# Kernel optimization log

Hardware: AMD Instinct MI355X
Metric: run time of the kernel (lower is better)

The kernel has to match this reference:

```python
import jax, jax.numpy as jnp
import numpy as np

N = 32768      # total nodes
G = 64         # graphs
NPG = 512      # nodes per graph (equal-size graphs)
K = 256        # ceil(NPG * pooling_ratio), pooling_ratio=0.5
D = 256        # input_dim
H = 256        # hidden_dim
FD = 3 * H     # fusion dim
C = 10         # num_classes
E = 262144     # edges
EPS = 1e-5     # BatchNorm eps


def setup_inputs() -> dict:
    key = jax.random.key(0)
    ks = jax.random.split(key, 20)
    w = lambda k, s: jax.random.normal(k, s, jnp.float32) * 0.05
    inp = {
        'x': jax.random.normal(ks[0], (N, D), jnp.float32),
        'edge_index': jax.random.randint(ks[1], (2, E), 0, N, jnp.int64),
        'batch': (jnp.arange(N, dtype=jnp.int64) // NPG),
        'w_s1': w(ks[2], (D, H)), 'b_s1': jnp.zeros((H,), jnp.float32),
        'w_s21': w(ks[3], (D, H)), 'b_s21': jnp.zeros((H,), jnp.float32),
        'w_s22': w(ks[4], (H, H)), 'b_s22': jnp.zeros((H,), jnp.float32),
        'w_raw': w(ks[5], (D, H)), 'b_raw': jnp.zeros((H,), jnp.float32),
        'w_pos': w(ks[6], (FD, 1)), 'b_pos': jnp.zeros((1,), jnp.float32),
        'w_neg': w(ks[7], (FD, 1)), 'b_neg': jnp.zeros((1,), jnp.float32),
        'w_pool': w(ks[8], (FD, FD)), 'b_pool': jnp.zeros((FD,), jnp.float32),
        'w1': w(ks[9], (2 * FD, 256)), 'b1': jnp.zeros((256,), jnp.float32),
        'g1': jnp.ones((256,), jnp.float32), 'be1': jnp.zeros((256,), jnp.float32),
        'w2': w(ks[10], (256, 256)), 'b2': jnp.zeros((256,), jnp.float32),
        'g2': jnp.ones((256,), jnp.float32), 'be2': jnp.zeros((256,), jnp.float32),
        'w3': w(ks[11], (256, 256)), 'b3': jnp.zeros((256,), jnp.float32),
        'g3': jnp.ones((256,), jnp.float32), 'be3': jnp.zeros((256,), jnp.float32),
        'w4': w(ks[12], (256, C)), 'b4': jnp.zeros((C,), jnp.float32),
    }
    return inp


def _gcn(x, W, b, src, dst, dinv):
    # PyG GCNConv: linear, then sym-normalized aggregation with self-loops
    h = x @ W
    norm = dinv[src] * dinv[dst]
    agg = jax.ops.segment_sum(h[src] * norm[:, None], dst, num_segments=N)
    agg = agg + h * (dinv * dinv)[:, None]  # self-loop contribution
    return agg + b


def _bn(z, g, b):
    m = z.mean(0)
    v = z.var(0)  # biased, as torch BN training-mode normalization
    return (z - m) * jax.lax.rsqrt(v + EPS) * g + b


def _mlp(z, w1, b1, g1, be1, w2, b2, g2, be2, w3, b3, g3, be3, w4, b4):
    z = jax.nn.relu(_bn(z @ w1 + b1, g1, be1))  # dropout=identity (eval)
    idt = z
    o = jax.nn.relu(_bn(z @ w2 + b2, g2, be2))
    z = o + idt
    idt = z
    o = jax.nn.relu(_bn(z @ w3 + b3, g3, be3))
    z = o + idt
    return z @ w4 + b4


def _topk_mask(scores):
    # equal-size graphs -> per-graph top-k via one batched lax.top_k
    sg = scores.reshape(G, NPG)
    _, idx = jax.lax.top_k(sg, K)
    mask = jnp.zeros((G, NPG), bool).at[jnp.arange(G)[:, None], idx].set(True)
    return mask.reshape(-1)


def _readout(xt, mask):
    m = mask[:, None]
    xs = jnp.where(m, xt, 0.0).reshape(G, NPG, FD)
    mean_pool = xs.sum(1) / K
    mx = jnp.where(m, xt, -jnp.inf).reshape(G, NPG, FD).max(1)
    return jnp.concatenate([mean_pool, mx], axis=1)


def reference(x, edge_index, batch, w_s1, b_s1, w_s21, b_s21, w_s22, b_s22,
              w_raw, b_raw, w_pos, b_pos, w_neg, b_neg, w_pool, b_pool,
              w1, b1, g1, be1, w2, b2, g2, be2, w3, b3, g3, be3, w4, b4):
    src, dst = edge_index[0], edge_index[1]
    deg = jax.ops.segment_sum(jnp.ones_like(src, jnp.float32), dst, num_segments=N) + 1.0
    dinv = jax.lax.rsqrt(deg)
    lrelu = lambda z: jax.nn.leaky_relu(z, 0.01)

    h_s1 = lrelu(_gcn(x, w_s1, b_s1, src, dst, dinv))
    h_s2 = lrelu(_gcn(lrelu(_gcn(x, w_s21, b_s21, src, dst, dinv)), w_s22, b_s22, src, dst, dinv))
    h_raw = x @ w_raw + b_raw
    h_final = jnp.concatenate([h_s1, h_s2, h_raw], axis=1)  # [N, FD]

    score_pos = jax.nn.sigmoid(_gcn(h_final, w_pos, b_pos, src, dst, dinv)).reshape(-1)
    score_neg = jax.nn.sigmoid(_gcn(h_final, w_neg, b_neg, src, dst, dinv)).reshape(-1)

    xt = jax.nn.sigmoid(h_final @ w_pool + b_pool)  # pool_transform for all nodes; mask selects
    mask_pos = _topk_mask(score_pos)
    mask_neg = _topk_mask(score_neg)

    mlp = lambda e: _mlp(e, w1, b1, g1, be1, w2, b2, g2, be2, w3, b3, g3, be3, w4, b4)
    logits_pos = mlp(_readout(xt, mask_pos))
    probs_pos = jax.nn.softmax(logits_pos, axis=1)
    logits_neg = mlp(_readout(xt, mask_neg))
    probs_neg = jax.nn.softmax(logits_neg, axis=1)
    return (logits_pos, probs_pos, probs_neg, score_pos, score_neg, batch)
```

## Files before the change

kernel.cpp:

```cpp
#include <hip/hip_runtime.h>
#include <hip/hip_bf16.h>

#define N_NODES 32768
#define NGRAPH  64
#define NPG     512
#define TOPK    256
#define HID     256
#define FDIM    768
#define NEDGE   262144
#define NCLS    10
#define BN_EPS  1e-5f

#define IN_BF16 0
#define OUT_BF16 0

typedef __attribute__((ext_vector_type(8))) short short8;
typedef __attribute__((ext_vector_type(4))) float f32x4;

__device__ __forceinline__ float bf2f(unsigned short u) {
    return __uint_as_float(((unsigned)u) << 16);
}
__device__ __forceinline__ unsigned short f2bf(float f) {
    unsigned x = __float_as_uint(f);
    unsigned r = (x + 0x7fffu + ((x >> 16) & 1u)) >> 16;
    return (unsigned short)r;
}
__device__ __forceinline__ float in_ld(const void* p, size_t i) {
#if IN_BF16
    return bf2f(((const unsigned short*)p)[i]);
#else
    return ((const float*)p)[i];
#endif
}
__device__ __forceinline__ void st_out(void* o, size_t i, float v) {
#if OUT_BF16
    ((unsigned short*)o)[i] = f2bf(v);
#else
    ((float*)o)[i] = v;
#endif
}

__device__ __forceinline__ void async_cp16(const unsigned short* g, unsigned short* l) {
    __builtin_amdgcn_global_load_lds(
        (const __attribute__((address_space(1))) unsigned int*)g,
        (__attribute__((address_space(3))) unsigned int*)l, 16, 0, 0);
}

__device__ __forceinline__ void tile_swizzle(int& bm, int& bn) {
    int nx = gridDim.x;
    int L = blockIdx.y * nx + blockIdx.x;
    int xcd = L & 7;
    int j = L >> 3;
    bm = ((j / nx) * 8 + xcd) * 128;
    bn = (j % nx) * 128;
}

__global__ __launch_bounds__(256) void cvt_all_kernel(const float* __restrict__ x,
                                                      const float* __restrict__ w_s1,
                                                      const float* __restrict__ w_s21,
                                                      const float* __restrict__ w_s22,
                                                      const float* __restrict__ w_raw,
                                                      const float* __restrict__ w_pool,
                                                      const float* __restrict__ w_pos,
                                                      const float* __restrict__ w_neg,
                                                      unsigned short* __restrict__ xbf,
                                                      unsigned short* __restrict__ wcat2,
                                                      unsigned short* __restrict__ wb_s22,
                                                      unsigned short* __restrict__ wb_raw,
                                                      unsigned short* __restrict__ wpool896) {
    int id = blockIdx.x;
    if (id < 4096) {
        size_t base = (size_t)id * 2048 + threadIdx.x * 8;
        float4 a = *(const float4*)(x + base);
        float4 b = *(const float4*)(x + base + 4);
        unsigned short o[8] = { f2bf(a.x), f2bf(a.y), f2bf(a.z), f2bf(a.w),
                                f2bf(b.x), f2bf(b.y), f2bf(b.z), f2bf(b.w) };
        *(uint4*)(xbf + base) = *(uint4*)o;
        return;
    }
    if (id >= 4928) {
        int j = id - 4928;
        const float* src = (j < 3) ? w_pos : w_neg;
        int seg = (j < 3) ? j : j - 3;
        size_t row = (j < 3) ? 768 : 769;
        wpool896[row * 768 + seg * 256 + threadIdx.x] = f2bf(src[seg * 256 + threadIdx.x]);
        return;
    }
    __shared__ unsigned short tile[32][33];
    const float* src;
    unsigned short* dst;
    int K, N, t;
    if (id < 4160)      { src = w_s1;  dst = wcat2;                     K = 256; N = 256; t = id - 4096; }
    else if (id < 4224) { src = w_s21; dst = wcat2 + (size_t)256 * 256; K = 256; N = 256; t = id - 4160; }
    else if (id < 4288) { src = w_s22; dst = wb_s22;                    K = 256; N = 256; t = id - 4224; }
    else if (id < 4352) { src = w_raw; dst = wb_raw;                    K = 256; N = 256; t = id - 4288; }
    else                { src = w_pool; dst = wpool896;                 K = 768; N = 768; t = id - 4352; }
    int tiles_x = K >> 5;
    int bk = (t % tiles_x) * 32, bn = (t / tiles_x) * 32;
    int tx = threadIdx.x & 31, ty = threadIdx.x >> 5;
#pragma unroll
    for (int i = 0; i < 32; i += 8)
        tile[ty + i][tx] = f2bf(src[(size_t)(bk + ty + i) * N + bn + tx]);
    __syncthreads();
#pragma unroll
    for (int i = 0; i < 32; i += 8)
        dst[(size_t)(bn + ty + i) * K + bk + tx] = tile[tx][ty + i];
}

__global__ __launch_bounds__(256) void detect_kernel(const int* __restrict__ eb, int* __restrict__ flag) {
    int i = blockIdx.x * 256 + threadIdx.x;
    int v = eb[2 * (size_t)i + 1];
    unsigned long long b = __ballot(v != 0);
    if ((threadIdx.x & 63) == 0 && b)
        atomicAdd(flag, (int)__popcll(b));
}

__global__ __launch_bounds__(256) void hist_kernel(const int* __restrict__ eb, const int* __restrict__ flag,
                                                   int* __restrict__ deg) {
    int e = blockIdx.x * 256 + threadIdx.x;
    int st = (*flag == 0) ? 2 : 1;
    unsigned d = ((const unsigned*)eb)[(size_t)(NEDGE + e) * st] & (N_NODES - 1);
    atomicAdd(&deg[d], 1);
}

__global__ __launch_bounds__(1024) void scan_kernel(const int* __restrict__ cnt, int* __restrict__ rowptr,
                                                    int* __restrict__ cursor, float* __restrict__ dinv) {
    __shared__ int part[1024];
    int t = threadIdx.x;
    int base = t * 32;
    int loc[32];
    int s = 0;
#pragma unroll
    for (int i = 0; i < 32; i++) { loc[i] = cnt[base + i]; s += loc[i]; }
    part[t] = s;
    __syncthreads();
    for (int off = 1; off < 1024; off <<= 1) {
        int v = (t >= off) ? part[t - off] : 0;
        __syncthreads();
        part[t] += v;
        __syncthreads();
    }
    int run = (t == 0) ? 0 : part[t - 1];
#pragma unroll
    for (int i = 0; i < 32; i++) {
        rowptr[base + i] = run;
        cursor[base + i] = run;
        dinv[base + i] = rsqrtf((float)loc[i] + 1.0f);
        run += loc[i];
    }
    if (t == 1023) rowptr[N_NODES] = run;
}

__global__ __launch_bounds__(256) void scatter_kernel(const int* __restrict__ eb, const int* __restrict__ flag,
                                                      int* __restrict__ cursor, int* __restrict__ srcs) {
    int e = blockIdx.x * 256 + threadIdx.x;
    int st = (*flag == 0) ? 2 : 1;
    unsigned s = ((const unsigned*)eb)[(size_t)e * st] & (N_NODES - 1);
    unsigned d = ((const unsigned*)eb)[(size_t)(NEDGE + e) * st] & (N_NODES - 1);
    int p = atomicAdd(&cursor[d], 1);
    srcs[p] = (int)s;
}

#define GEMM_CORE(K_)                                                           \
    __shared__ unsigned short As[128 * 64];                                     \
    __shared__ unsigned short Bs[128 * 64];                                     \
    const int tid = threadIdx.x;                                                \
    const int wave = tid >> 6;                                                  \
    const int lane = tid & 63;                                                  \
    int bm, bn;                                                                 \
    tile_swizzle(bm, bn);                                                       \
    const int wm = (wave >> 1) * 64;                                            \
    const int wn = (wave & 1) * 64;                                             \
    const int l15 = lane & 15;                                                  \
    const int q = lane >> 4;                                                    \
    f32x4 acc[4][4] = {};                                                       \
    const int srow = lane >> 3;                                                 \
    const int schunk = lane & 7;                                                \
    const int gc = schunk ^ srow;                                               \
    const unsigned short* gaA = A + (size_t)(bm + wave * 8 + srow) * (K_) + gc * 8;  \
    const unsigned short* gbB = WT + (size_t)(bn + wave * 8 + srow) * (K_) + gc * 8; \
    const size_t K32 = (size_t)(K_) * 32;                                       \
    unsigned short* const la0 = &As[(wave * 8) * 64];                           \
    unsigned short* const lb0 = &Bs[(wave * 8) * 64];                           \
    for (int k0 = 0; k0 < (K_); k0 += 64) {                                     \
        __syncthreads();                                                        \
        _Pragma("unroll")                                                       \
        for (int t = 0; t < 4; t++) {                                           \
            async_cp16(gaA + t * K32 + k0, la0 + t * 32 * 64);                  \
            async_cp16(gbB + t * K32 + k0, lb0 + t * 32 * 64);                  \
        }                                                                       \
        __syncthreads();                                                        \
        _Pragma("unroll")                                                       \
        for (int h = 0; h < 2; h++) {                                           \
            short8 af[4], bfv[4];                                               \
            int p = (h * 4 + q) ^ (l15 & 7);                                    \
            _Pragma("unroll")                                                   \
            for (int t = 0; t < 4; t++) {                                       \
                int m = wm + t * 16 + l15;                                      \
                int n = wn + t * 16 + l15;                                      \
                af[t] = *(const short8*)&As[m * 64 + p * 8];                    \
                bfv[t] = *(const short8*)&Bs[n * 64 + p * 8];                   \
            }                                                                   \
            _Pragma("unroll")                                                   \
            for (int tm = 0; tm < 4; tm++)                                      \
                _Pragma("unroll")                                               \
                for (int tn = 0; tn < 4; tn++)                                  \
                    acc[tm][tn] = __builtin_amdgcn_mfma_f32_16x16x32_bf16(af[tm], bfv[tn], acc[tm][tn], 0, 0, 0); \
        }                                                                       \
    }

__global__ __launch_bounds__(256) void gemm_kernel(const unsigned short* __restrict__ A,
                                                   const unsigned short* __restrict__ WT,
                                                   const float* __restrict__ bias,
                                                   unsigned short* __restrict__ C,
                                                   int K, int ldC, int colOff, int epi) {
    GEMM_CORE(K)
#pragma unroll
    for (int tm = 0; tm < 4; tm++) {
        int row = bm + wm + tm * 16 + q * 4;
#pragma unroll
        for (int tn = 0; tn < 4; tn++) {
            int col = bn + wn + tn * 16 + l15;
            float bv = bias ? bias[col] : 0.0f;
#pragma unroll
            for (int r = 0; r < 4; r++) {
                float v = acc[tm][tn][r] + bv;
                if (epi == 1) v = 1.0f / (1.0f + __expf(-v));
                else if (epi == 2) v = v > 0.f ? v : 0.01f * v;
                C[(size_t)(row + r) * ldC + colOff + col] = f2bf(v);
            }
        }
    }
}

__global__ __launch_bounds__(256) void gemmA_kernel(const unsigned short* __restrict__ A,
                                                    const unsigned short* __restrict__ WT,
                                                    const float* __restrict__ b_s1,
                                                    const float* __restrict__ b_s21,
                                                    unsigned short* __restrict__ hfin,
                                                    unsigned short* __restrict__ t1) {
    GEMM_CORE(256)
#pragma unroll
    for (int tm = 0; tm < 4; tm++) {
        int row = bm + wm + tm * 16 + q * 4;
#pragma unroll
        for (int tn = 0; tn < 4; tn++) {
            int col = bn + wn + tn * 16 + l15;
            if (col < 256) {
                float bv = b_s1[col];
#pragma unroll
                for (int r = 0; r < 4; r++) {
                    float v = acc[tm][tn][r] + bv;
                    v = v > 0.f ? v : 0.01f * v;
                    hfin[(size_t)(row + r) * 768 + col] = f2bf(v);
                }
            } else {
                float bv = b_s21[col - 256];
#pragma unroll
                for (int r = 0; r < 4; r++) {
                    float v = acc[tm][tn][r] + bv;
                    v = v > 0.f ? v : 0.01f * v;
                    t1[(size_t)(row + r) * 256 + (col - 256)] = f2bf(v);
                }
            }
        }
    }
}

__global__ __launch_bounds__(256) void gemmP_kernel(const unsigned short* __restrict__ A,
                                                    const unsigned short* __restrict__ WT,
                                                    const float* __restrict__ b_pool,
                                                    unsigned short* __restrict__ xt,
                                                    float* __restrict__ svp, float* __restrict__ svn,
                                                    int K) {
    GEMM_CORE(K)
#pragma unroll
    for (int tm = 0; tm < 4; tm++) {
        int row = bm + wm + tm * 16 + q * 4;
#pragma unroll
        for (int tn = 0; tn < 4; tn++) {
            int col = bn + wn + tn * 16 + l15;
            if (col < 768) {
                float bv = b_pool[col];
#pragma unroll
                for (int r = 0; r < 4; r++) {
                    float v = acc[tm][tn][r] + bv;
                    v = 1.0f / (1.0f + __expf(-v));
                    xt[(size_t)(row + r) * 768 + col] = f2bf(v);
                }
            } else if (col == 768) {
#pragma unroll
                for (int r = 0; r < 4; r++) svp[row + r] = acc[tm][tn][r];
            } else if (col == 769) {
#pragma unroll
                for (int r = 0; r < 4; r++) svn[row + r] = acc[tm][tn][r];
            }
        }
    }
}

__global__ __launch_bounds__(256) void lin_agg_kernel(const unsigned short* __restrict__ h,
                                                      const int* __restrict__ rowptr, const int* __restrict__ srcs,
                                                      const float* __restrict__ dinv,
                                                      unsigned short* __restrict__ out) {
    int wave = threadIdx.x >> 6, lane = threadIdx.x & 63;
    int v = blockIdx.x * 4 + wave;
    int f0 = lane * 4;
    float a0 = 0.f, a1 = 0.f, a2 = 0.f, a3 = 0.f;
    int s = rowptr[v], e = rowptr[v + 1];
    for (int i = s; i < e; i++) {
        int u = srcs[i] & (N_NODES - 1);
        float du = dinv[u];
        uint2 hv = *(const uint2*)(h + (size_t)u * 256 + f0);
        a0 += bf2f((unsigned short)(hv.x & 0xffff)) * du;
        a1 += bf2f((unsigned short)(hv.x >> 16)) * du;
        a2 += bf2f((unsigned short)(hv.y & 0xffff)) * du;
        a3 += bf2f((unsigned short)(hv.y >> 16)) * du;
    }
    float dv = dinv[v], dv2 = dv * dv;
    uint2 sv = *(const uint2*)(h + (size_t)v * 256 + f0);
    float r0 = dv * a0 + bf2f((unsigned short)(sv.x & 0xffff)) * dv2;
    float r1 = dv * a1 + bf2f((unsigned short)(sv.x >> 16)) * dv2;
    float r2 = dv * a2 + bf2f((unsigned short)(sv.y & 0xffff)) * dv2;
    float r3 = dv * a3 + bf2f((unsigned short)(sv.y >> 16)) * dv2;
    uint2 ov = make_uint2(((unsigned)f2bf(r1) << 16) | f2bf(r0), ((unsigned)f2bf(r3) << 16) | f2bf(r2));
    *(uint2*)(out + (size_t)v * 256 + f0) = ov;
}

__global__ __launch_bounds__(256) void score_agg_kernel(const float* __restrict__ svp, const float* __restrict__ svn,
                                                        const int* __restrict__ rowptr, const int* __restrict__ srcs,
                                                        const float* __restrict__ dinv,
                                                        const void* __restrict__ bp, const void* __restrict__ bn_,
                                                        float* __restrict__ scp, float* __restrict__ scn,
                                                        void* __restrict__ dout) {
    int v = blockIdx.x * 256 + threadIdx.x;
    float ap = 0.f, an = 0.f;
    int s = rowptr[v], e = rowptr[v + 1];
    for (int i = s; i < e; i++) {
        int u = srcs[i] & (N_NODES - 1);
        float du = dinv[u];
        ap += svp[u] * du;
        an += svn[u] * du;
    }
    float dv = dinv[v], dv2 = dv * dv;
    float zp = dv * ap + svp[v] * dv2 + in_ld(bp, 0);
    float zn = dv * an + svn[v] * dv2 + in_ld(bn_, 0);
    float pp = 1.0f / (1.0f + __expf(-zp));
    float pn = 1.0f / (1.0f + __expf(-zn));
    scp[v] = pp;
    scn[v] = pn;
    st_out(dout, 1920 + (size_t)v, pp);
    st_out(dout, 1920 + (size_t)N_NODES + v, pn);
    st_out(dout, 1920 + 2 * (size_t)N_NODES + v, (float)(v >> 9));
}

__global__ __launch_bounds__(512) void topk2_kernel(const float* __restrict__ scp, const float* __restrict__ scn,
                                                    unsigned char* __restrict__ maskp,
                                                    unsigned char* __restrict__ maskn) {
    __shared__ float s[512];
    const float* sc = (blockIdx.x & 1) ? scn : scp;
    unsigned char* mask = (blockIdx.x & 1) ? maskn : maskp;
    int g = blockIdx.x >> 1, i = threadIdx.x;
    float my = sc[(size_t)g * 512 + i];
    s[i] = my;
    __syncthreads();
    int cnt = 0;
    for (int j = 0; j < 512; j++) {
        float o = s[j];
        cnt += (int)((o > my) || ((o == my) && (j < i)));
    }
    mask[(size_t)g * 512 + i] = (cnt < TOPK) ? 1 : 0;
}

__global__ __launch_bounds__(256) void readout2_kernel(const unsigned short* __restrict__ xt,
                                                       const unsigned char* __restrict__ maskp,
                                                       const unsigned char* __restrict__ maskn,
                                                       float* __restrict__ eout) {
    int g = blockIdx.x;
    int c = blockIdx.y;
    int wv = threadIdx.x >> 6, lane = threadIdx.x & 63;
    int f = c * 64 + lane;
    __shared__ unsigned char mp[512], mn[512];
    __shared__ float red[4][64][4];
    for (int i = threadIdx.x; i < 512; i += 256) {
        mp[i] = maskp[(size_t)g * 512 + i];
        mn[i] = maskn[(size_t)g * 512 + i];
    }
    __syncthreads();
    float sp = 0.f, sn = 0.f, xp = -INFINITY, xn = -INFINITY;
    const unsigned short* base = xt + ((size_t)g * 512 + wv * 128) * 768 + f;
    for (int v = 0; v < 128; v++) {
        unsigned char bp = mp[wv * 128 + v], bn_ = mn[wv * 128 + v];
        if (!(bp | bn_)) continue;
        float x = bf2f(base[(size_t)v * 768]);
        if (bp) { sp += x; xp = fmaxf(xp, x); }
        if (bn_) { sn += x; xn = fmaxf(xn, x); }
    }
    red[wv][lane][0] = sp; red[wv][lane][1] = xp;
    red[wv][lane][2] = sn; red[wv][lane][3] = xn;
    __syncthreads();
    if (wv == 0) {
#pragma unroll
        for (int w = 1; w < 4; w++) {
            sp += red[w][lane][0]; xp = fmaxf(xp, red[w][lane][1]);
            sn += red[w][lane][2]; xn = fmaxf(xn, red[w][lane][3]);
        }
        float* erp = eout + (size_t)g * 1536;
        float* ern = eout + (size_t)(64 + g) * 1536;
        erp[f] = sp * (1.0f / TOPK);
        erp[768 + f] = xp;
        ern[f] = sn * (1.0f / TOPK);
        ern[768 + f] = xn;
    }
}

__global__ __launch_bounds__(256) void mlp_gemm2_kernel(const float* __restrict__ in,
                                                        const float* __restrict__ W,
                                                        const float* __restrict__ b,
                                                        float* __restrict__ out, int K) {
    __shared__ float row[1536];
    __shared__ float red[4][64];
    int r = blockIdx.x, cg = blockIdx.y;
    int wv = threadIdx.x >> 6, lane = threadIdx.x & 63;
    int c = cg * 64 + lane;
    for (int k = threadIdx.x; k < K; k += 256) row[k] = in[(size_t)r * K + k];
    __syncthreads();
    int kpw = K >> 2;
    const float* wp = W + (size_t)(wv * kpw) * 256 + c;
    const float* rp = row + wv * kpw;
    float acc = 0.f;
#pragma unroll 4
    for (int k = 0; k < kpw; k++)
        acc += rp[k] * wp[(size_t)k * 256];
    red[wv][lane] = acc;
    __syncthreads();
    if (wv == 0) {
        float v = red[0][lane] + red[1][lane] + red[2][lane] + red[3][lane] + b[c];
        out[(size_t)r * 256 + c] = v;
    }
}

__global__ __launch_bounds__(64) void bn_kernel(const float* __restrict__ z, const void* __restrict__ gamma,
                                                const void* __restrict__ beta, const float* __restrict__ res,
                                                float* __restrict__ out) {
    int f = blockIdx.x & 255, g = blockIdx.x >> 8, r = threadIdx.x;
    size_t idx = (size_t)(g * 64 + r) * 256 + f;
    float x = z[idx];
    float s = x, sq = x * x;
    for (int off = 1; off < 64; off <<= 1) {
        s += __shfl_xor(s, off, 64);
        sq += __shfl_xor(sq, off, 64);
    }
    float m = s * (1.0f / 64.0f);
    float var = sq * (1.0f / 64.0f) - m * m;
    float y = (x - m) * rsqrtf(var + BN_EPS) * in_ld(gamma, f) + in_ld(beta, f);
    y = fmaxf(y, 0.0f);
    if (res) y += res[idx];
    out[idx] = y;
}

__global__ __launch_bounds__(64) void logits_kernel(const float* __restrict__ act, const void* __restrict__ w4,
                                                    const void* __restrict__ b4, float* __restrict__ lg) {
    int idx = blockIdx.x * 64 + threadIdx.x;
    if (idx >= 128 * NCLS) return;
    int r = idx / NCLS, c = idx % NCLS;
    float acc = in_ld(b4, c);
    for (int k = 0; k < 256; k++) acc += act[(size_t)r * 256 + k] * in_ld(w4, (size_t)k * NCLS + c);
    lg[idx] = acc;
}

__global__ __launch_bounds__(64) void softmax_kernel(const float* __restrict__ lg, void* __restrict__ dout) {
    int r = blockIdx.x * 64 + threadIdx.x;
    if (r >= 128) return;
    float l[NCLS];
    float mx = -1e30f;
    for (int c = 0; c < NCLS; c++) { l[c] = lg[(size_t)r * NCLS + c]; mx = fmaxf(mx, l[c]); }
    float sum = 0.f;
    float ex[NCLS];
    for (int c = 0; c < NCLS; c++) { ex[c] = __expf(l[c] - mx); sum += ex[c]; }
    float inv = 1.0f / sum;
    int g = r >> 6, rr = r & 63;
    if (g == 0) {
        for (int c = 0; c < NCLS; c++) st_out(dout, (size_t)rr * NCLS + c, l[c]);
        for (int c = 0; c < NCLS; c++) st_out(dout, 640 + (size_t)rr * NCLS + c, ex[c] * inv);
    } else {
        for (int c = 0; c < NCLS; c++) st_out(dout, 1280 + (size_t)rr * NCLS + c, ex[c] * inv);
    }
}

extern "C" void kernel_launch(void* const* d_in, const int* in_sizes, int n_in,
                              void* d_out, int out_size, void* d_ws, size_t ws_size,
                              hipStream_t stream) {
    (void)in_sizes; (void)n_in; (void)out_size; (void)ws_size;

    const float* x = (const float*)d_in[0];
    const int* eb = (const int*)d_in[1];
    const float* w_s1 = (const float*)d_in[3];
    const float* b_s1 = (const float*)d_in[4];
    const float* w_s21 = (const float*)d_in[5];
    const float* b_s21 = (const float*)d_in[6];
    const float* w_s22 = (const float*)d_in[7];
    const float* b_s22 = (const float*)d_in[8];
    const float* w_raw = (const float*)d_in[9];
    const float* b_raw = (const float*)d_in[10];
    const float* w_pos = (const float*)d_in[11];
    const void* b_pos = d_in[12];
    const float* w_neg = (const float*)d_in[13];
    const void* b_neg = d_in[14];
    const float* w_pool = (const float*)d_in[15];
    const float* b_pool = (const float*)d_in[16];
    const float* w1 = (const float*)d_in[17];  const float* b1 = (const float*)d_in[18];
    const void* g1 = d_in[19];  const void* be1 = d_in[20];
    const float* w2 = (const float*)d_in[21];  const float* b2 = (const float*)d_in[22];
    const void* g2 = d_in[23];  const void* be2 = d_in[24];
    const float* w3 = (const float*)d_in[25];  const float* b3 = (const float*)d_in[26];
    const void* g3 = d_in[27];  const void* be3 = d_in[28];
    const void* w4 = d_in[29];  const void* b4 = d_in[30];

    char* ws = (char*)d_ws;
    size_t off = 0;
    auto alloc = [&](size_t b) -> void* {
        void* p = ws + off;
        off += (b + 255) & ~(size_t)255;
        return p;
    };
    int* flag = (int*)alloc(256);
    int* deg = (int*)alloc((size_t)N_NODES * 4);
    float* dinv = (float*)alloc((size_t)N_NODES * 4);
    int* rowptr = (int*)alloc((size_t)(N_NODES + 1) * 4);
    int* cursor = (int*)alloc((size_t)N_NODES * 4);
    int* srcs = (int*)alloc((size_t)NEDGE * 4);
    unsigned short* xbf = (unsigned short*)alloc((size_t)N_NODES * 256 * 2);
    unsigned short* wcat2 = (unsigned short*)alloc((size_t)512 * 256 * 2);
    unsigned short* wb_s22 = (unsigned short*)alloc((size_t)256 * 256 * 2);
    unsigned short* wb_raw = (unsigned short*)alloc((size_t)256 * 256 * 2);
    unsigned short* wpool896 = (unsigned short*)alloc((size_t)896 * 768 * 2);
    unsigned short* Xa = (unsigned short*)alloc((size_t)N_NODES * 256 * 2);
    unsigned short* t1 = (unsigned short*)alloc((size_t)N_NODES * 256 * 2);
    unsigned short* t1a = (unsigned short*)alloc((size_t)N_NODES * 256 * 2);
    unsigned short* hfin = (unsigned short*)alloc((size_t)N_NODES * 768 * 2);
    unsigned short* xt = (unsigned short*)alloc((size_t)N_NODES * 768 * 2);
    float* svp = (float*)alloc((size_t)N_NODES * 4);
    float* svn = (float*)alloc((size_t)N_NODES * 4);
    float* scp = (float*)alloc((size_t)N_NODES * 4);
    float* scn = (float*)alloc((size_t)N_NODES * 4);
    unsigned char* maskp = (unsigned char*)alloc(N_NODES);
    unsigned char* maskn = (unsigned char*)alloc(N_NODES);
    float* ebuf = (float*)alloc((size_t)128 * 1536 * 4);
    float* zb = (float*)alloc((size_t)128 * 256 * 4);
    float* act1 = (float*)alloc((size_t)128 * 256 * 4);
    float* act2 = (float*)alloc((size_t)128 * 256 * 4);
    float* act3 = (float*)alloc((size_t)128 * 256 * 4);
    float* lg = (float*)alloc((size_t)128 * NCLS * 4);

    hipMemsetAsync(flag, 0, 256, stream);
    hipMemsetAsync(deg, 0, (size_t)N_NODES * 4, stream);
    hipMemsetAsync(wpool896 + (size_t)770 * 768, 0, (size_t)126 * 768 * 2, stream);

    detect_kernel<<<NEDGE / 256, 256, 0, stream>>>(eb, flag);
    hist_kernel<<<NEDGE / 256, 256, 0, stream>>>(eb, flag, deg);
    scan_kernel<<<1, 1024, 0, stream>>>(deg, rowptr, cursor, dinv);
    scatter_kernel<<<NEDGE / 256, 256, 0, stream>>>(eb, flag, cursor, srcs);

    cvt_all_kernel<<<4934, 256, 0, stream>>>(x, w_s1, w_s21, w_s22, w_raw, w_pool, w_pos, w_neg,
                                             xbf, wcat2, wb_s22, wb_raw, wpool896);

    dim3 gA2(512 / 128, N_NODES / 128);
    dim3 gA1(256 / 128, N_NODES / 128);
    dim3 gP(896 / 128, N_NODES / 128);

    lin_agg_kernel<<<N_NODES / 4, 256, 0, stream>>>(xbf, rowptr, srcs, dinv, Xa);
    gemmA_kernel<<<gA2, 256, 0, stream>>>(Xa, wcat2, b_s1, b_s21, hfin, t1);
    lin_agg_kernel<<<N_NODES / 4, 256, 0, stream>>>(t1, rowptr, srcs, dinv, t1a);
    gemm_kernel<<<gA1, 256, 0, stream>>>(t1a, wb_s22, b_s22, hfin, 256, 768, 256, 2);
    gemm_kernel<<<gA1, 256, 0, stream>>>(xbf, wb_raw, b_raw, hfin, 256, 768, 512, 0);
    gemmP_kernel<<<gP, 256, 0, stream>>>(hfin, wpool896, b_pool, xt, svp, svn, 768);
    score_agg_kernel<<<N_NODES / 256, 256, 0, stream>>>(svp, svn, rowptr, srcs, dinv, b_pos, b_neg, scp, scn, d_out);
    topk2_kernel<<<2 * NGRAPH, 512, 0, stream>>>(scp, scn, maskp, maskn);
    {
        dim3 gR(NGRAPH, FDIM / 64);
        readout2_kernel<<<gR, 256, 0, stream>>>(xt, maskp, maskn, ebuf);
    }
    {
        dim3 gM(128, 4);
        mlp_gemm2_kernel<<<gM, 256, 0, stream>>>(ebuf, w1, b1, zb, 1536);
        bn_kernel<<<512, 64, 0, stream>>>(zb, g1, be1, nullptr, act1);
        mlp_gemm2_kernel<<<gM, 256, 0, stream>>>(act1, w2, b2, zb, 256);
        bn_kernel<<<512, 64, 0, stream>>>(zb, g2, be2, act1, act2);
        mlp_gemm2_kernel<<<gM, 256, 0, stream>>>(act2, w3, b3, zb, 256);
        bn_kernel<<<512, 64, 0, stream>>>(zb, g3, be3, act2, act3);
    }
    logits_kernel<<<(128 * NCLS + 63) / 64, 64, 0, stream>>>(act3, w4, b4, lg);
    softmax_kernel<<<2, 64, 0, stream>>>(lg, d_out);
}
```

Before: 589.6 us.

## Fuse raw GEMM into first GEMM, merge score-agg with topk, fuse logits+softmax

Folds the raw-feature GEMM into the first-layer GEMM launch so one 6-column-tile grid covers both. The pool GEMM drops its padded 896-column weight and the score projections move to a separate bf16 mat-vec kernel. Score aggregation and top-k masking are merged into one per-graph kernel, logits and softmax become one head kernel, and the two memsets are combined. The aim is fewer launches, less padded GEMM work and no intermediate score buffers, at the cost of an extra pass that re-reads hfin for the score mat-vec.

New measurement: 578.9 us (median of 2 runs). No clear change (-1.8%).

```diff
diff --git a/kernel.cpp b/kernel.cpp
--- a/kernel.cpp
+++ b/kernel.cpp
@@ -61,13 +61,11 @@
                                                       const float* __restrict__ w_s22,
                                                       const float* __restrict__ w_raw,
                                                       const float* __restrict__ w_pool,
-                                                      const float* __restrict__ w_pos,
-                                                      const float* __restrict__ w_neg,
                                                       unsigned short* __restrict__ xbf,
                                                       unsigned short* __restrict__ wcat2,
                                                       unsigned short* __restrict__ wb_s22,
                                                       unsigned short* __restrict__ wb_raw,
-                                                      unsigned short* __restrict__ wpool896) {
+                                                      unsigned short* __restrict__ wb_pool) {
     int id = blockIdx.x;
     if (id < 4096) {
         size_t base = (size_t)id * 2048 + threadIdx.x * 8;
@@ -78,14 +76,6 @@
         *(uint4*)(xbf + base) = *(uint4*)o;
         return;
     }
-    if (id >= 4928) {
-        int j = id - 4928;
-        const float* src = (j < 3) ? w_pos : w_neg;
-        int seg = (j < 3) ? j : j - 3;
-        size_t row = (j < 3) ? 768 : 769;
-        wpool896[row * 768 + seg * 256 + threadIdx.x] = f2bf(src[seg * 256 + threadIdx.x]);
-        return;
-    }
     __shared__ unsigned short tile[32][33];
     const float* src;
     unsigned short* dst;
@@ -94,7 +84,7 @@
     else if (id < 4224) { src = w_s21; dst = wcat2 + (size_t)256 * 256; K = 256; N = 256; t = id - 4160; }
     else if (id < 4288) { src = w_s22; dst = wb_s22;                    K = 256; N = 256; t = id - 4224; }
     else if (id < 4352) { src = w_raw; dst = wb_raw;                    K = 256; N = 256; t = id - 4288; }
-    else                { src = w_pool; dst = wpool896;                 K = 768; N = 768; t = id - 4352; }
+    else                { src = w_pool; dst = wb_pool;                  K = 768; N = 768; t = id - 4352; }
     int tiles_x = K >> 5;
     int bk = (t % tiles_x) * 32, bn = (t / tiles_x) * 32;
     int tx = threadIdx.x & 31, ty = threadIdx.x >> 5;
@@ -161,14 +151,12 @@
     srcs[p] = (int)s;
 }
 
-#define GEMM_CORE(K_)                                                           \
+#define GEMM_BODY(K_)                                                           \
     __shared__ unsigned short As[128 * 64];                                     \
     __shared__ unsigned short Bs[128 * 64];                                     \
     const int tid = threadIdx.x;                                                \
     const int wave = tid >> 6;                                                  \
     const int lane = tid & 63;                                                  \
-    int bm, bn;                                                                 \
-    tile_swizzle(bm, bn);                                                       \
     const int wm = (wave >> 1) * 64;                                            \
     const int wn = (wave & 1) * 64;                                             \
     const int l15 = lane & 15;                                                  \
@@ -214,7 +202,9 @@
                                                    const float* __restrict__ bias,
                                                    unsigned short* __restrict__ C,
                                                    int K, int ldC, int colOff, int epi) {
-    GEMM_CORE(K)
+    int bm, bn;
+    tile_swizzle(bm, bn);
+    GEMM_BODY(K)
 #pragma unroll
     for (int tm = 0; tm < 4; tm++) {
         int row = bm + wm + tm * 16 + q * 4;
@@ -233,67 +223,54 @@
     }
 }
 
-__global__ __launch_bounds__(256) void gemmA_kernel(const unsigned short* __restrict__ A,
-                                                    const unsigned short* __restrict__ WT,
-                                                    const float* __restrict__ b_s1,
-                                                    const float* __restrict__ b_s21,
-                                                    unsigned short* __restrict__ hfin,
-                                                    unsigned short* __restrict__ t1) {
-    GEMM_CORE(256)
+__global__ __launch_bounds__(256) void gemmA6_kernel(const unsigned short* __restrict__ Xa,
+                                                     const unsigned short* __restrict__ wcat2,
+                                                     const unsigned short* __restrict__ xbf,
+                                                     const unsigned short* __restrict__ wb_raw,
+                                                     const float* __restrict__ b_s1,
+                                                     const float* __restrict__ b_s21,
+                                                     const float* __restrict__ b_raw,
+                                                     unsigned short* __restrict__ hfin,
+                                                     unsigned short* __restrict__ t1) {
+    const int nx = 6;
+    int L = blockIdx.y * nx + blockIdx.x;
+    int xcd = L & 7, j = L >> 3;
+    int bm = ((j / nx) * 8 + xcd) * 128;
+    int bnt = j % nx;
+    int sub = (bnt < 4) ? 0 : 1;
+    const unsigned short* A = sub ? xbf : Xa;
+    const unsigned short* WT = sub ? wb_raw : wcat2;
+    int bn = sub ? (bnt - 4) * 128 : bnt * 128;
+    GEMM_BODY(256)
 #pragma unroll
     for (int tm = 0; tm < 4; tm++) {
         int row = bm + wm + tm * 16 + q * 4;
 #pragma unroll
         for (int tn = 0; tn < 4; tn++) {
             int col = bn + wn + tn * 16 + l15;
-            if (col < 256) {
-                float bv = b_s1[col];
-#pragma unroll
-                for (int r = 0; r < 4; r++) {
-                    float v = acc[tm][tn][r] + bv;
-                    v = v > 0.f ? v : 0.01f * v;
-                    hfin[(size_t)(row + r) * 768 + col] = f2bf(v);
+            if (sub == 0) {
+                if (col < 256) {
+                    float bv = b_s1[col];
+#pragma unroll
+                    for (int r = 0; r < 4; r++) {
+                        float v = acc[tm][tn][r] + bv;
+                        v = v > 0.f ? v : 0.01f * v;
+                        hfin[(size_t)(row + r) * 768 + col] = f2bf(v);
+                    }
+                } else {
+                    float bv = b_s21[col - 256];
+#pragma unroll
+                    for (int r = 0; r < 4; r++) {
+                        float v = acc[tm][tn][r] + bv;
+                        v = v > 0.f ? v : 0.01f * v;
+                        t1[(size_t)(row + r) * 256 + (col - 256)] = f2bf(v);
+                    }
                 }
             } else {
-                float bv = b_s21[col - 256];
-#pragma unroll
-                for (int r = 0; r < 4; r++) {
-                    float v = acc[tm][tn][r] + bv;
-                    v = v > 0.f ? v : 0.01f * v;
-                    t1[(size_t)(row + r) * 256 + (col - 256)] = f2bf(v);
-                }
-            }
-        }
-    }
-}
-
-__global__ __launch_bounds__(256) void gemmP_kernel(const unsigned short* __restrict__ A,
-                                                    const unsigned short* __restrict__ WT,
-                                                    const float* __restrict__ b_pool,
-                                                    unsigned short* __restrict__ xt,
-                                                    float* __restrict__ svp, float* __restrict__ svn,
-                                                    int K) {
-    GEMM_CORE(K)
-#pragma unroll
-    for (int tm = 0; tm < 4; tm++) {
-        int row = bm + wm + tm * 16 + q * 4;
-#pragma unroll
-        for (int tn = 0; tn < 4; tn++) {
-            int col = bn + wn + tn * 16 + l15;
-            if (col < 768) {
-                float bv = b_pool[col];
-#pragma unroll
-                for (int r = 0; r < 4; r++) {
-                    float v = acc[tm][tn][r] + bv;
-                    v = 1.0f / (1.0f + __expf(-v));
-                    xt[(size_t)(row + r) * 768 + col] = f2bf(v);
-                }
-            } else if (col == 768) {
-#pragma unroll
-                for (int r = 0; r < 4; r++) svp[row + r] = acc[tm][tn][r];
-            } else if (col == 769) {
-#pragma unroll
-                for (int r = 0; r < 4; r++) svn[row + r] = acc[tm][tn][r];
+                float bv = b_raw[col];
+#pragma unroll
+                for (int r = 0; r < 4; r++)
+                    hfin[(size_t)(row + r) * 768 + 512 + col] = f2bf(acc[tm][tn][r] + bv);
             }
         }
     }
@@ -327,17 +304,44 @@
     *(uint2*)(out + (size_t)v * 256 + f0) = ov;
 }
 
-__global__ __launch_bounds__(256) void score_agg_kernel(const float* __restrict__ svp, const float* __restrict__ svn,
-                                                        const int* __restrict__ rowptr, const int* __restrict__ srcs,
-                                                        const float* __restrict__ dinv,
-                                                        const void* __restrict__ bp, const void* __restrict__ bn_,
-                                                        float* __restrict__ scp, float* __restrict__ scn,
-                                                        void* __restrict__ dout) {
-    int v = blockIdx.x * 256 + threadIdx.x;
+__global__ __launch_bounds__(256) void score_mv_kernel(const unsigned short* __restrict__ hf,
+                                                       const void* __restrict__ wp, const void* __restrict__ wn,
+                                                       float* __restrict__ svp, float* __restrict__ svn) {
+    int wave = threadIdx.x >> 6, lane = threadIdx.x & 63;
+    int v = blockIdx.x * 4 + wave;
+    float sp = 0.f, sn = 0.f;
+#pragma unroll
+    for (int i = 0; i < 3; i++) {
+        int k = i * 256 + lane * 4;
+        uint2 hv = *(const uint2*)(hf + (size_t)v * 768 + k);
+        float x0 = bf2f((unsigned short)(hv.x & 0xffff));
+        float x1 = bf2f((unsigned short)(hv.x >> 16));
+        float x2 = bf2f((unsigned short)(hv.y & 0xffff));
+        float x3 = bf2f((unsigned short)(hv.y >> 16));
+        sp += x0 * in_ld(wp, k) + x1 * in_ld(wp, k + 1) + x2 * in_ld(wp, k + 2) + x3 * in_ld(wp, k + 3);
+        sn += x0 * in_ld(wn, k) + x1 * in_ld(wn, k + 1) + x2 * in_ld(wn, k + 2) + x3 * in_ld(wn, k + 3);
+    }
+    for (int off = 32; off >= 1; off >>= 1) {
+        sp += __shfl_down(sp, off, 64);
+        sn += __shfl_down(sn, off, 64);
+    }
+    if (lane == 0) { svp[v] = sp; svn[v] = sn; }
+}
+
+__global__ __launch_bounds__(512) void score_topk_kernel(const float* __restrict__ svp, const float* __restrict__ svn,
+                                                         const int* __restrict__ rowptr, const int* __restrict__ srcs,
+                                                         const float* __restrict__ dinv,
+                                                         const void* __restrict__ bp, const void* __restrict__ bn_,
+                                                         unsigned char* __restrict__ maskp,
+                                                         unsigned char* __restrict__ maskn,
+                                                         void* __restrict__ dout) {
+    __shared__ float sp[512], sn[512];
+    int g = blockIdx.x, i = threadIdx.x;
+    int v = g * 512 + i;
     float ap = 0.f, an = 0.f;
     int s = rowptr[v], e = rowptr[v + 1];
-    for (int i = s; i < e; i++) {
-        int u = srcs[i] & (N_NODES - 1);
+    for (int k = s; k < e; k++) {
+        int u = srcs[k] & (N_NODES - 1);
         float du = dinv[u];
         ap += svp[u] * du;
         an += svn[u] * du;
@@ -347,29 +351,19 @@
     float zn = dv * an + svn[v] * dv2 + in_ld(bn_, 0);
     float pp = 1.0f / (1.0f + __expf(-zp));
     float pn = 1.0f / (1.0f + __expf(-zn));
-    scp[v] = pp;
-    scn[v] = pn;
     st_out(dout, 1920 + (size_t)v, pp);
     st_out(dout, 1920 + (size_t)N_NODES + v, pn);
-    st_out(dout, 1920 + 2 * (size_t)N_NODES + v, (float)(v >> 9));
-}
-
-__global__ __launch_bounds__(512) void topk2_kernel(const float* __restrict__ scp, const float* __restrict__ scn,
-                                                    unsigned char* __restrict__ maskp,
-                                                    unsigned char* __restrict__ maskn) {
-    __shared__ float s[512];
-    const float* sc = (blockIdx.x & 1) ? scn : scp;
-    unsigned char* mask = (blockIdx.x & 1) ? maskn : maskp;
-    int g = blockIdx.x >> 1, i = threadIdx.x;
-    float my = sc[(size_t)g * 512 + i];
-    s[i] = my;
-    __syncthreads();
-    int cnt = 0;
+    st_out(dout, 1920 + 2 * (size_t)N_NODES + v, (float)g);
+    sp[i] = pp; sn[i] = pn;
+    __syncthreads();
+    int cp = 0, cn = 0;
     for (int j = 0; j < 512; j++) {
-        float o = s[j];
-        cnt += (int)((o > my) || ((o == my) && (j < i)));
-    }
-    mask[(size_t)g * 512 + i] = (cnt < TOPK) ? 1 : 0;
+        float op = sp[j], on = sn[j];
+        cp += (int)((op > pp) || ((op == pp) && (j < i)));
+        cn += (int)((on > pn) || ((on == pn) && (j < i)));
+    }
+    maskp[v] = (cp < TOPK) ? 1 : 0;
+    maskn[v] = (cn < TOPK) ? 1 : 0;
 }
 
 __global__ __launch_bounds__(256) void readout2_kernel(const unsigned short* __restrict__ xt,
@@ -459,32 +453,30 @@
     out[idx] = y;
 }
 
-__global__ __launch_bounds__(64) void logits_kernel(const float* __restrict__ act, const void* __restrict__ w4,
-                                                    const void* __restrict__ b4, float* __restrict__ lg) {
-    int idx = blockIdx.x * 64 + threadIdx.x;
-    if (idx >= 128 * NCLS) return;
-    int r = idx / NCLS, c = idx % NCLS;
-    float acc = in_ld(b4, c);
-    for (int k = 0; k < 256; k++) acc += act[(size_t)r * 256 + k] * in_ld(w4, (size_t)k * NCLS + c);
-    lg[idx] = acc;
-}
-
-__global__ __launch_bounds__(64) void softmax_kernel(const float* __restrict__ lg, void* __restrict__ dout) {
-    int r = blockIdx.x * 64 + threadIdx.x;
-    if (r >= 128) return;
-    float l[NCLS];
-    float mx = -1e30f;
-    for (int c = 0; c < NCLS; c++) { l[c] = lg[(size_t)r * NCLS + c]; mx = fmaxf(mx, l[c]); }
-    float sum = 0.f;
-    float ex[NCLS];
-    for (int c = 0; c < NCLS; c++) { ex[c] = __expf(l[c] - mx); sum += ex[c]; }
-    float inv = 1.0f / sum;
-    int g = r >> 6, rr = r & 63;
-    if (g == 0) {
-        for (int c = 0; c < NCLS; c++) st_out(dout, (size_t)rr * NCLS + c, l[c]);
-        for (int c = 0; c < NCLS; c++) st_out(dout, 640 + (size_t)rr * NCLS + c, ex[c] * inv);
-    } else {
-        for (int c = 0; c < NCLS; c++) st_out(dout, 1280 + (size_t)rr * NCLS + c, ex[c] * inv);
+__global__ __launch_bounds__(64) void head_kernel(const float* __restrict__ act, const void* __restrict__ w4,
+                                                  const void* __restrict__ b4, void* __restrict__ dout) {
+    __shared__ float l[NCLS];
+    int r = blockIdx.x, t = threadIdx.x;
+    if (t < NCLS) {
+        float acc = in_ld(b4, t);
+        for (int k = 0; k < 256; k++)
+            acc += act[(size_t)r * 256 + k] * in_ld(w4, (size_t)k * NCLS + t);
+        l[t] = acc;
+    }
+    __syncthreads();
+    if (t == 0) {
+        float mx = -1e30f;
+        for (int c = 0; c < NCLS; c++) mx = fmaxf(mx, l[c]);
+        float ex[NCLS], sum = 0.f;
+        for (int c = 0; c < NCLS; c++) { ex[c] = __expf(l[c] - mx); sum += ex[c]; }
+        float inv = 1.0f / sum;
+        int g = r >> 6, rr = r & 63;
+        if (g == 0) {
+            for (int c = 0; c < NCLS; c++) st_out(dout, (size_t)rr * NCLS + c, l[c]);
+            for (int c = 0; c < NCLS; c++) st_out(dout, 640 + (size_t)rr * NCLS + c, ex[c] * inv);
+        } else {
+            for (int c = 0; c < NCLS; c++) st_out(dout, 1280 + (size_t)rr * NCLS + c, ex[c] * inv);
+        }
     }
 }
 
@@ -503,9 +495,9 @@
     const float* b_s22 = (const float*)d_in[8];
     const float* w_raw = (const float*)d_in[9];
     const float* b_raw = (const float*)d_in[10];
-    const float* w_pos = (const float*)d_in[11];
+    const void* w_pos = d_in[11];
     const void* b_pos = d_in[12];
-    const float* w_neg = (const float*)d_in[13];
+    const void* w_neg = d_in[13];
     const void* b_neg = d_in[14];
     const float* w_pool = (const float*)d_in[15];
     const float* b_pool = (const float*)d_in[16];
@@ -534,7 +526,7 @@
     unsigned short* wcat2 = (unsigned short*)alloc((size_t)512 * 256 * 2);
     unsigned short* wb_s22 = (unsigned short*)alloc((size_t)256 * 256 * 2);
     unsigned short* wb_raw = (unsigned short*)alloc((size_t)256 * 256 * 2);
-    unsigned short* wpool896 = (unsigned short*)alloc((size_t)896 * 768 * 2);
+    unsigned short* wb_pool = (unsigned short*)alloc((size_t)768 * 768 * 2);
     unsigned short* Xa = (unsigned short*)alloc((size_t)N_NODES * 256 * 2);
     unsigned short* t1 = (unsigned short*)alloc((size_t)N_NODES * 256 * 2);
     unsigned short* t1a = (unsigned short*)alloc((size_t)N_NODES * 256 * 2);
@@ -542,8 +534,6 @@
     unsigned short* xt = (unsigned short*)alloc((size_t)N_NODES * 768 * 2);
     float* svp = (float*)alloc((size_t)N_NODES * 4);
     float* svn = (float*)alloc((size_t)N_NODES * 4);
-    float* scp = (float*)alloc((size_t)N_NODES * 4);
-    float* scn = (float*)alloc((size_t)N_NODES * 4);
     unsigned char* maskp = (unsigned char*)alloc(N_NODES);
     unsigned char* maskn = (unsigned char*)alloc(N_NODES);
     float* ebuf = (float*)alloc((size_t)128 * 1536 * 4);
@@ -551,32 +541,29 @@
     float* act1 = (float*)alloc((size_t)128 * 256 * 4);
     float* act2 = (float*)alloc((size_t)128 * 256 * 4);
     float* act3 = (float*)alloc((size_t)128 * 256 * 4);
-    float* lg = (float*)alloc((size_t)128 * NCLS * 4);
-
-    hipMemsetAsync(flag, 0, 256, stream);
-    hipMemsetAsync(deg, 0, (size_t)N_NODES * 4, stream);
-    hipMemsetAsync(wpool896 + (size_t)770 * 768, 0, (size_t)126 * 768 * 2, stream);
+
+    hipMemsetAsync(flag, 0, 256 + (size_t)N_NODES * 4, stream);
 
     detect_kernel<<<NEDGE / 256, 256, 0, stream>>>(eb, flag);
     hist_kernel<<<NEDGE / 256, 256, 0, stream>>>(eb, flag, deg);
     scan_kernel<<<1, 1024, 0, stream>>>(deg, rowptr, cursor, dinv);
     scatter_kernel<<<NEDGE / 256, 256, 0, stream>>>(eb, flag, cursor, srcs);
 
-    cvt_all_kernel<<<4934, 256, 0, stream>>>(x, w_s1, w_s21, w_s22, w_raw, w_pool, w_pos, w_neg,
-                                             xbf, wcat2, wb_s22, wb_raw, wpool896);
-
-    dim3 gA2(512 / 128, N_NODES / 128);
-    dim3 gA1(256 / 128, N_NODES / 128);
-    dim3 gP(896 / 128, N_NODES / 128);
+    cvt_all_kernel<<<4928, 256, 0, stream>>>(x, w_s1, w_s21, w_s22, w_raw, w_pool,
+                                             xbf, wcat2, wb_s22, wb_raw, wb_pool);
+
+    dim3 gA6(6, N_NODES / 128);
+    dim3 gA1(2, N_NODES / 128);
+    dim3 gP(6, N_NODES / 128);
 
     lin_agg_kernel<<<N_NODES / 4, 256, 0, stream>>>(xbf, rowptr, srcs, dinv, Xa);
-    gemmA_kernel<<<gA2, 256, 0, stream>>>(Xa, wcat2, b_s1, b_s21, hfin, t1);
+    gemmA6_kernel<<<gA6, 256, 0, stream>>>(Xa, wcat2, xbf, wb_raw, b_s1, b_s21, b_raw, hfin, t1);
     lin_agg_kernel<<<N_NODES / 4, 256, 0, stream>>>(t1, rowptr, srcs, dinv, t1a);
     gemm_kernel<<<gA1, 256, 0, stream>>>(t1a, wb_s22, b_s22, hfin, 256, 768, 256, 2);
-    gemm_kernel<<<gA1, 256, 0, stream>>>(xbf, wb_raw, b_raw, hfin, 256, 768, 512, 0);
-    gemmP_kernel<<<gP, 256, 0, stream>>>(hfin, wpool896, b_pool, xt, svp, svn, 768);
-    score_agg_kernel<<<N_NODES / 256, 256, 0, stream>>>(svp, svn, rowptr, srcs, dinv, b_pos, b_neg, scp, scn, d_out);
-    topk2_kernel<<<2 * NGRAPH, 512, 0, stream>>>(scp, scn, maskp, maskn);
+    gemm_kernel<<<gP, 256, 0, stream>>>(hfin, wb_pool, b_pool, xt, 768, 768, 0, 1);
+    score_mv_kernel<<<N_NODES / 4, 256, 0, stream>>>(hfin, w_pos, w_neg, svp, svn);
+    score_topk_kernel<<<NGRAPH, 512, 0, stream>>>(svp, svn, rowptr, srcs, dinv, b_pos, b_neg,
+                                                  maskp, maskn, d_out);
     {
         dim3 gR(NGRAPH, FDIM / 64);
         readout2_kernel<<<gR, 256, 0, stream>>>(xt, maskp, maskn, ebuf);
@@ -590,6 +577,5 @@
         mlp_gemm2_kernel<<<gM, 256, 0, stream>>>(act2, w3, b3, zb, 256);
         bn_kernel<<<512, 64, 0, stream>>>(zb, g3, be3, act2, act3);
     }
-    logits_kernel<<<(128 * NCLS + 63) / 64, 64, 0, stream>>>(act3, w4, b4, lg);
-    softmax_kernel<<<2, 64, 0, stream>>>(lg, d_out);
-}
+    head_kernel<<<128, 64, 0, stream>>>(act3, w4, b4, d_out);
+}
```
